# Kernel tuning notes

Hardware: AMD Instinct MI355X
Metric: run time of the kernel (lower is better)

The kernel has to match this reference:

```python
import jax, jax.numpy as jnp
import numpy as np

B, S, D = 4, 1024, 2048
H, KVH, HD = 32, 8, 64
N_REP = H // KVH  # 4
ROPE_THETA = 1000000.0


def _rope_tables(seq_len, head_dim, theta):
    inv_freq = 1.0 / (theta ** (np.arange(0, head_dim, 2, dtype=np.float32) / head_dim))
    t = np.arange(seq_len, dtype=np.float32)
    freqs = np.outer(t, inv_freq)                      # (S, HD/2)
    emb = np.concatenate([freqs, freqs], axis=-1)      # (S, HD)
    return jnp.asarray(np.cos(emb)), jnp.asarray(np.sin(emb))


def setup_inputs() -> dict:
    key = jax.random.key(0)
    kx, kq, kk, kv, ko = jax.random.split(key, 5)
    cos, sin = _rope_tables(S, HD, ROPE_THETA)
    s = 0.02
    return {
        "x": jax.random.normal(kx, (B, S, D), jnp.float32),
        "cos": cos,
        "sin": sin,
        "Wq": jax.random.normal(kq, (D, H * HD), jnp.float32) * s,
        "Wk": jax.random.normal(kk, (D, KVH * HD), jnp.float32) * s,
        "Wv": jax.random.normal(kv, (D, KVH * HD), jnp.float32) * s,
        "Wo": jax.random.normal(ko, (H * HD, D), jnp.float32) * s,
    }


def _rotate_half(t):
    t1, t2 = jnp.split(t, 2, axis=-1)
    return jnp.concatenate([-t2, t1], axis=-1)


def reference(x, cos, sin, Wq, Wk, Wv, Wo):
    # projections
    q = (x @ Wq).reshape(B, S, H, HD)      # (b, s, h, d)
    k = (x @ Wk).reshape(B, S, KVH, HD)
    v = (x @ Wv).reshape(B, S, KVH, HD)

    # RoPE: cos/sin (s, d) broadcast over heads (unsqueeze_dim=1 -> (s,1,d))
    c = cos[:, None, :]
    sn = sin[:, None, :]
    q = q * c + _rotate_half(q) * sn
    k = k * c + _rotate_half(k) * sn

    # GQA attention without physically repeating KV:
    # q grouped as (b, kvh, n_rep, s, d); repeat_kv '(h r)' maps q head g*n_rep+r -> kv head g
    qg = q.transpose(0, 2, 1, 3).reshape(B, KVH, N_REP, S, HD)
    kt = k.transpose(0, 2, 1, 3)  # (b, kvh, s, d)
    vt = v.transpose(0, 2, 1, 3)

    scale = 1.0 / jnp.sqrt(jnp.asarray(HD, x.dtype))
    scores = jnp.einsum('bgrqd,bgkd->bgrqk', qg, kt) * scale  # (b, kvh, rep, s, s)
    probs = jax.nn.softmax(scores, axis=-1)
    out = jnp.einsum('bgrqk,bgkd->bgrqd', probs, vt)           # (b, kvh, rep, s, d)

    out = out.reshape(B, H, S, HD).transpose(0, 2, 1, 3).reshape(B, S, H * HD)
    return out @ Wo
```

## Files before the change

### kernel.cpp

```cpp
#include <hip/hip_runtime.h>

typedef unsigned short u16;
typedef __attribute__((ext_vector_type(8))) __bf16 bf16x8;
typedef __attribute__((ext_vector_type(4))) _Float16 f16x4;
typedef __attribute__((ext_vector_type(8))) _Float16 f16x8;
typedef __attribute__((ext_vector_type(4))) float f32x4;

#define BB 4
#define SS 1024
#define DD 2048
#define HH 32
#define KVHN 8
#define HDIM 64

__device__ __forceinline__ u16 f2b(float f) {
    union { float f; unsigned u; } v; v.f = f;
    unsigned r = v.u + 0x7FFFu + ((v.u >> 16) & 1u);
    return (u16)(r >> 16);
}
__device__ __forceinline__ float b2f(u16 h) {
    union { unsigned u; float f; } v; v.u = ((unsigned)h) << 16; return v.f;
}

__device__ __forceinline__ f32x4 mfma16(bf16x8 a, bf16x8 b, f32x4 c) {
    return __builtin_amdgcn_mfma_f32_16x16x32_bf16(a, b, c, 0, 0, 0);
}
__device__ __forceinline__ f32x4 mfma16h(f16x8 a, f16x8 b, f32x4 c) {
    return __builtin_amdgcn_mfma_f32_16x16x32_f16(a, b, c, 0, 0, 0);
}

__device__ __forceinline__ void async_cp16(const void* g, void* l) {
    __builtin_amdgcn_global_load_lds((__attribute__((address_space(1))) void*)g,
                                     (__attribute__((address_space(3))) void*)l,
                                     16, 0, 0);
}

__device__ __forceinline__ void block_sync() {
    asm volatile("" ::: "memory");
    __builtin_amdgcn_s_barrier();
    asm volatile("" ::: "memory");
}

__device__ __forceinline__ f16x8 pack8_f16(const float* p) {
    union { unsigned u[4]; f16x8 v; } pu;
    pu.u[0] = __builtin_bit_cast(unsigned, __builtin_amdgcn_cvt_pkrtz(p[0], p[1]));
    pu.u[1] = __builtin_bit_cast(unsigned, __builtin_amdgcn_cvt_pkrtz(p[2], p[3]));
    pu.u[2] = __builtin_bit_cast(unsigned, __builtin_amdgcn_cvt_pkrtz(p[4], p[5]));
    pu.u[3] = __builtin_bit_cast(unsigned, __builtin_amdgcn_cvt_pkrtz(p[6], p[7]));
    return pu.v;
}

__global__ __launch_bounds__(256) void cast_x_kernel(const float* __restrict__ x,
                                                     u16* __restrict__ xb) {
    int i = (blockIdx.x * 256 + threadIdx.x) * 4;
    float4 v = *(const float4*)(x + i);
    unsigned r0 = (unsigned)f2b(v.x) | ((unsigned)f2b(v.y) << 16);
    unsigned r1 = (unsigned)f2b(v.z) | ((unsigned)f2b(v.w) << 16);
    *(uint2*)(xb + i) = make_uint2(r0, r1);
}

__global__ __launch_bounds__(256) void wtrans_all_kernel(const float* __restrict__ Wq,
                                                         const float* __restrict__ Wk,
                                                         const float* __restrict__ Wv,
                                                         const float* __restrict__ Wo,
                                                         u16* __restrict__ Wqkvt,
                                                         u16* __restrict__ Wot) {
    __shared__ float tile[32][33];
    int z = blockIdx.z;
    const float* W = (z == 0) ? Wq : (z == 1) ? Wk : (z == 2) ? Wv : Wo;
    int N = (z == 1 || z == 2) ? 512 : 2048;
    int n_off = (z == 1) ? 2048 : (z == 2) ? 2560 : 0;
    u16* Wt = (z == 3) ? Wot : Wqkvt;
    int n0 = blockIdx.x * 32;
    if (n0 >= N) return;
    int k0 = blockIdx.y * 32;
    int tid = threadIdx.x;
    int nj = tid & 31;
    int ki = tid >> 5;
#pragma unroll
    for (int it = 0; it < 4; it++) {
        int kk = it * 8 + ki;
        tile[kk][nj] = W[(size_t)(k0 + kk) * N + n0 + nj];
    }
    __syncthreads();
#pragma unroll
    for (int it = 0; it < 4; it++) {
        int nn = it * 8 + ki;
        Wt[(size_t)(n0 + nn + n_off) * 2048 + k0 + nj] = f2b(tile[nj][nn]);
    }
}

__global__ __launch_bounds__(512, 2) void gemm_qkv(const u16* __restrict__ A,
                                                   const u16* __restrict__ Bt,
                                                   u16* __restrict__ C) {
    __shared__ __align__(16) u16 Ls[4][16384];
    const int tid = threadIdx.x;
    const int lane = tid & 63;
    const int w = tid >> 6;
    const int m0 = blockIdx.y * 256;
    const int n0 = blockIdx.x * 256;
    const int wm = (w >> 2) * 128;
    const int wn = (w & 3) * 64;
    const int lr = lane & 15;
    const int lg = lane >> 4;

    const int srow = w * 16 + (lane >> 2);
    const int sg = (lane & 3) ^ ((srow >> 1) & 3);
    const u16* ap = A + (size_t)(m0 + srow) * 2048 + sg * 8;
    const u16* bp = Bt + (size_t)(n0 + srow) * 2048 + sg * 8;

#define QSTAGE_A(pb_, kt_)                                                       \
    {                                                                            \
        async_cp16(ap + (kt_) * 32, &Ls[pb_][0] + w * 512);                      \
        async_cp16(ap + (kt_) * 32 + 128 * 2048, &Ls[pb_][4096] + w * 512);      \
    }
#define QSTAGE_B(pb_, kt_)                                                       \
    {                                                                            \
        async_cp16(bp + (kt_) * 32, &Ls[pb_][8192] + w * 512);                   \
        async_cp16(bp + (kt_) * 32 + 128 * 2048, &Ls[pb_][12288] + w * 512);     \
    }

    f32x4 acc[8][4];
    const f32x4 zero4 = {0.f, 0.f, 0.f, 0.f};
#pragma unroll
    for (int i = 0; i < 8; i++)
#pragma unroll
        for (int j = 0; j < 4; j++) acc[i][j] = zero4;

    QSTAGE_A(0, 0); QSTAGE_B(0, 0);
    QSTAGE_A(1, 1); QSTAGE_B(1, 1);
    QSTAGE_A(2, 2); QSTAGE_B(2, 2);
    asm volatile("s_waitcnt vmcnt(8)" ::: "memory");
    block_sync();

#pragma unroll 4
    for (int t = 0; t < 64; ++t) {
        const int bufi = t & 3;
        const int pb = (t + 3) & 3;
        const int pt = (t + 3) & 63;
        const u16* Ab = &Ls[bufi][0];
        const u16* Bb = &Ls[bufi][8192];

        bf16x8 af[4], bfr[4];
#pragma unroll
        for (int ni = 0; ni < 4; ni++) {
            int r = wn + ni * 16 + lr;
            bfr[ni] = *(const bf16x8*)(Bb + r * 32 + ((lg ^ ((r >> 1) & 3)) * 8));
        }
#pragma unroll
        for (int mi = 0; mi < 4; mi++) {
            int r = wm + mi * 16 + lr;
            af[mi] = *(const bf16x8*)(Ab + r * 32 + ((lg ^ ((r >> 1) & 3)) * 8));
        }
        QSTAGE_A(pb, pt);
        __builtin_amdgcn_s_setprio(1);
#pragma unroll
        for (int mi = 0; mi < 4; mi++)
#pragma unroll
            for (int ni = 0; ni < 4; ni++)
                acc[mi][ni] = mfma16(af[mi], bfr[ni], acc[mi][ni]);
        __builtin_amdgcn_s_setprio(0);

#pragma unroll
        for (int mi = 0; mi < 4; mi++) {
            int r = wm + 64 + mi * 16 + lr;
            af[mi] = *(const bf16x8*)(Ab + r * 32 + ((lg ^ ((r >> 1) & 3)) * 8));
        }
        QSTAGE_B(pb, pt);
        __builtin_amdgcn_s_setprio(1);
#pragma unroll
        for (int mi = 0; mi < 4; mi++)
#pragma unroll
            for (int ni = 0; ni < 4; ni++)
                acc[4 + mi][ni] = mfma16(af[mi], bfr[ni], acc[4 + mi][ni]);
        __builtin_amdgcn_s_setprio(0);

        asm volatile("s_waitcnt vmcnt(8)" ::: "memory");
        block_sync();
    }
    asm volatile("s_waitcnt vmcnt(0)" ::: "memory");

    const int lq = lg * 4;
#pragma unroll
    for (int mi = 0; mi < 8; mi++)
#pragma unroll
        for (int ni = 0; ni < 4; ni++)
#pragma unroll
            for (int i = 0; i < 4; i++) {
                int r = m0 + wm + mi * 16 + lq + i;
                int c = n0 + wn + ni * 16 + lr;
                C[(size_t)r * 3072 + c] = f2b(acc[mi][ni][i]);
            }
#undef QSTAGE_A
#undef QSTAGE_B
}

__global__ __launch_bounds__(512, 2) void gemm_out(const u16* __restrict__ A,
                                                   const u16* __restrict__ Bt,
                                                   float* __restrict__ C) {
    __shared__ __align__(16) u16 Ls[4][12288];
    const int tid = threadIdx.x;
    const int lane = tid & 63;
    const int w = tid >> 6;
    const int m0 = blockIdx.y * 256;
    const int n0 = blockIdx.x * 128;
    const int wm = (w >> 1) * 64;
    const int wn = (w & 1) * 64;
    const int lr = lane & 15;
    const int lg = lane >> 4;

    const int srow = w * 16 + (lane >> 2);
    const int sg = (lane & 3) ^ ((srow >> 1) & 3);
    const u16* ap = A + (size_t)(m0 + srow) * 2048 + sg * 8;
    const u16* bp = Bt + (size_t)(n0 + srow) * 2048 + sg * 8;

#define OSTAGE(pb_, kt_)                                                         \
    {                                                                            \
        async_cp16(ap + (kt_) * 32, &Ls[pb_][0] + w * 512);                      \
        async_cp16(ap + (kt_) * 32 + 128 * 2048, &Ls[pb_][4096] + w * 512);      \
        async_cp16(bp + (kt_) * 32, &Ls[pb_][8192] + w * 512);                   \
    }

    f32x4 acc[4][4];
    const f32x4 zero4 = {0.f, 0.f, 0.f, 0.f};
#pragma unroll
    for (int i = 0; i < 4; i++)
#pragma unroll
        for (int j = 0; j < 4; j++) acc[i][j] = zero4;

    OSTAGE(0, 0);
    OSTAGE(1, 1);
    OSTAGE(2, 2);
    asm volatile("s_waitcnt vmcnt(6)" ::: "memory");
    block_sync();

#pragma unroll 4
    for (int t = 0; t < 64; ++t) {
        const int bufi = t & 3;
        const int pb = (t + 3) & 3;
        const int pt = (t + 3) & 63;
        const u16* Ab = &Ls[bufi][0];
        const u16* Bb = &Ls[bufi][8192];

        bf16x8 af[4], bfr[4];
#pragma unroll
        for (int ni = 0; ni < 4; ni++) {
            int r = wn + ni * 16 + lr;
            bfr[ni] = *(const bf16x8*)(Bb + r * 32 + ((lg ^ ((r >> 1) & 3)) * 8));
        }
#pragma unroll
        for (int mi = 0; mi < 4; mi++) {
            int r = wm + mi * 16 + lr;
            af[mi] = *(const bf16x8*)(Ab + r * 32 + ((lg ^ ((r >> 1) & 3)) * 8));
        }
        OSTAGE(pb, pt);
        __builtin_amdgcn_s_setprio(1);
#pragma unroll
        for (int mi = 0; mi < 4; mi++)
#pragma unroll
            for (int ni = 0; ni < 4; ni++)
                acc[mi][ni] = mfma16(af[mi], bfr[ni], acc[mi][ni]);
        __builtin_amdgcn_s_setprio(0);

        asm volatile("s_waitcnt vmcnt(6)" ::: "memory");
        block_sync();
    }
    asm volatile("s_waitcnt vmcnt(0)" ::: "memory");

    const int lq = lg * 4;
#pragma unroll
    for (int mi = 0; mi < 4; mi++)
#pragma unroll
        for (int ni = 0; ni < 4; ni++)
#pragma unroll
            for (int i = 0; i < 4; i++) {
                int r = m0 + wm + mi * 16 + lq + i;
                int c = n0 + wn + ni * 16 + lr;
                C[(size_t)r * 2048 + c] = acc[mi][ni][i];
            }
#undef OSTAGE
}

__global__ __launch_bounds__(256) void rope_kernel(const u16* __restrict__ QKV,
                                                   const float* __restrict__ cosT,
                                                   const float* __restrict__ sinT,
                                                   u16* __restrict__ Qh,
                                                   u16* __restrict__ Kh) {
    const float QSC = 0.125f * 1.44269504088896f;
    int idx = blockIdx.x * 256 + threadIdx.x;
    int d = idx & 31;
    int t = idx >> 5;
    int hh = t % 40;
    int row = t / 40;
    int s = row & (SS - 1);
    int b = row >> 10;
    float c = cosT[s * HDIM + d];
    float sn = sinT[s * HDIM + d];
    if (hh < 32) {
        const u16* src = QKV + (size_t)row * 3072 + hh * 64 + d;
        float x1 = b2f(src[0]), x2 = b2f(src[32]);
        u16* dst = Qh + ((size_t)(b * HH + hh) * SS + s) * 64 + d;
        dst[0] = f2b((x1 * c - x2 * sn) * QSC);
        dst[32] = f2b((x2 * c + x1 * sn) * QSC);
    } else {
        int g = hh - 32;
        const u16* src = QKV + (size_t)row * 3072 + 2048 + g * 64 + d;
        float x1 = b2f(src[0]), x2 = b2f(src[32]);
        int rr = s & 7;
        int kpos = (s & ~31) + ((rr >= 4) ? 16 : 0) + ((s >> 3) & 3) * 4 + (rr & 3);
        u16* dst = Kh + ((size_t)(b * KVHN + g) * SS + kpos) * 64 + d;
        dst[0] = f2b(x1 * c - x2 * sn);
        dst[32] = f2b(x2 * c + x1 * sn);
    }
}

__global__ __launch_bounds__(256) void vtrans_kernel(const u16* __restrict__ QKV,
                                                     u16* __restrict__ Vt) {
    __shared__ u16 tile[64][65];
    int blk = blockIdx.x;
    int st = blk & 15;
    int t2 = blk >> 4;
    int g = t2 & 7;
    int b = t2 >> 3;
    int tid = threadIdx.x;
    int cj = tid & 63;
    int ri = tid >> 6;
    const u16* src = QKV + ((size_t)(b * SS + st * 64)) * 3072 + 2560 + g * 64;
#pragma unroll
    for (int it = 0; it < 16; it++) {
        int s_i = it * 4 + ri;
        tile[s_i][cj] = src[(size_t)s_i * 3072 + cj];
    }
    __syncthreads();
    u16* dst = Vt + ((size_t)(b * KVHN + g) * HDIM) * SS + st * 64;
#pragma unroll
    for (int it = 0; it < 16; it++) {
        int hd_i = it * 4 + ri;
        _Float16 hv = (_Float16)b2f(tile[cj][hd_i]);
        union { _Float16 h; u16 u; } cv; cv.h = hv;
        dst[(size_t)hd_i * SS + cj] = cv.u;
    }
}

__global__ __launch_bounds__(256, 4) void flash_kernel(const u16* __restrict__ Qh,
                                                       const u16* __restrict__ Kh,
                                                       const u16* __restrict__ Vt,
                                                       u16* __restrict__ Attn) {
    __shared__ __align__(16) u16 Kls[2][4096];
    __shared__ __align__(16) u16 Vls[2][4096];
    const int tid = threadIdx.x;
    const int lane = tid & 63;
    const int w = tid >> 6;
    const int qt = blockIdx.x;
    const int g = blockIdx.y;
    const int b = blockIdx.z;
    const int h = g * 4 + w;
    const int lr = lane & 15;
    const int lg = lane >> 4;
    const int lk8 = lg * 8;
    const int lq = lg * 4;

    const u16* Qbase = Qh + ((size_t)(b * HH + h) * SS + qt * 32) * HDIM;
    bf16x8 qb[2][2];
#pragma unroll
    for (int j = 0; j < 2; j++) {
        qb[j][0] = *(const bf16x8*)(Qbase + (size_t)(j * 16 + lr) * HDIM + lk8);
        qb[j][1] = *(const bf16x8*)(Qbase + (size_t)(j * 16 + lr) * HDIM + 32 + lk8);
    }

    const u16* Kbase = Kh + (size_t)(b * KVHN + g) * SS * HDIM;
    const u16* Vbase = Vt + (size_t)(b * KVHN + g) * HDIM * SS;

    const int r0 = tid >> 3;
    const int c0 = tid & 7;

    const f32x4 zero4 = {0.f, 0.f, 0.f, 0.f};
    const f32x4 initS = {-4.f, -4.f, -4.f, -4.f};
    f32x4 o[2][4];
    float lsum[2] = {0.f, 0.f};
#pragma unroll
    for (int j = 0; j < 2; j++)
#pragma unroll
        for (int i = 0; i < 4; i++) o[j][i] = zero4;

#define STAGE(kt, p)                                                              \
    {                                                                             \
        _Pragma("unroll") for (int sh = 0; sh < 2; sh++) {                        \
            int rr = r0 + sh * 32;                                                \
            int cs = c0 ^ (rr & 7);                                               \
            async_cp16(Kbase + (size_t)((kt) + rr) * HDIM + cs * 8,               \
                       &Kls[p][sh * 2048 + w * 512]);                             \
            async_cp16(Vbase + (size_t)rr * SS + (kt) + cs * 8,                   \
                       &Vls[p][sh * 2048 + w * 512]);                             \
        }                                                                         \
    }

    STAGE(0, 0);
    __syncthreads();

    for (int t = 0; t < 16; t++) {
        const int p = t & 1;
        if (t < 15) STAGE((t + 1) * 64, p ^ 1);

#pragma unroll
        for (int c = 0; c < 2; c++) {
            f32x4 s[2][2];
#pragma unroll
            for (int halfi = 0; halfi < 2; halfi++) {
                const int R = c * 32 + halfi * 16 + lr;
                const u16* kr = &Kls[p][R * 64];
                bf16x8 kb0 = *(const bf16x8*)(kr + ((lg ^ (R & 7)) * 8));
                bf16x8 kb1 = *(const bf16x8*)(kr + (((4 + lg) ^ (R & 7)) * 8));
#pragma unroll
                for (int j = 0; j < 2; j++) {
                    f32x4 a = initS;
                    a = mfma16(kb0, qb[j][0], a);
                    a = mfma16(kb1, qb[j][1], a);
                    s[halfi][j] = a;
                }
            }

            f16x8 va[4];
#pragma unroll
            for (int hdt = 0; hdt < 4; hdt++) {
                const int R2 = hdt * 16 + lr;
                va[hdt] = *(const f16x8*)(&Vls[p][R2 * 64 + (((c * 4 + lg) ^ (R2 & 7)) * 8)]);
            }

#pragma unroll
            for (int j = 0; j < 2; j++) {
                float pv[8];
#pragma unroll
                for (int r = 0; r < 4; r++) {
                    pv[r] = __builtin_amdgcn_exp2f(s[0][j][r]);
                    pv[4 + r] = __builtin_amdgcn_exp2f(s[1][j][r]);
                }
                lsum[j] += ((pv[0] + pv[1]) + (pv[2] + pv[3])) +
                           ((pv[4] + pv[5]) + (pv[6] + pv[7]));
                f16x8 pb = pack8_f16(pv);
#pragma unroll
                for (int hdt = 0; hdt < 4; hdt++)
                    o[j][hdt] = mfma16h(va[hdt], pb, o[j][hdt]);
            }
        }
        __syncthreads();
    }

#pragma unroll
    for (int j = 0; j < 2; j++) {
        float su = lsum[j];
        su += __shfl_xor(su, 16);
        su += __shfl_xor(su, 32);
        float inv = 1.f / su;
        u16* Ob = Attn + ((size_t)(b * SS + qt * 32 + j * 16 + lr)) * 2048 + h * 64;
#pragma unroll
        for (int hdt = 0; hdt < 4; hdt++) {
            unsigned r0p = (unsigned)f2b(o[j][hdt][0] * inv) | ((unsigned)f2b(o[j][hdt][1] * inv) << 16);
            unsigned r1p = (unsigned)f2b(o[j][hdt][2] * inv) | ((unsigned)f2b(o[j][hdt][3] * inv) << 16);
            *(uint2*)(Ob + hdt * 16 + lq) = make_uint2(r0p, r1p);
        }
    }
}

extern "C" void kernel_launch(void* const* d_in, const int* in_sizes, int n_in,
                              void* d_out, int out_size, void* d_ws, size_t ws_size,
                              hipStream_t stream) {
    (void)in_sizes; (void)n_in; (void)out_size; (void)ws_size;
    const float* x = (const float*)d_in[0];
    const float* cosT = (const float*)d_in[1];
    const float* sinT = (const float*)d_in[2];
    const float* Wq = (const float*)d_in[3];
    const float* Wk = (const float*)d_in[4];
    const float* Wv = (const float*)d_in[5];
    const float* Wo = (const float*)d_in[6];
    float* out = (float*)d_out;

    char* ws = (char*)d_ws;
    u16* Xb    = (u16*)(ws);
    u16* Wqkvt = (u16*)(ws + 16777216);
    u16* Wot   = (u16*)(ws + 29360128);
    u16* QKV   = (u16*)(ws + 37748736);
    u16* Qh    = (u16*)(ws + 62914560);
    u16* Kh    = (u16*)(ws + 79691776);
    u16* Vt    = (u16*)(ws + 83886080);
    u16* Attn  = (u16*)(ws + 88080384);

    cast_x_kernel<<<8192, 256, 0, stream>>>(x, Xb);
    wtrans_all_kernel<<<dim3(64, 64, 4), 256, 0, stream>>>(Wq, Wk, Wv, Wo, Wqkvt, Wot);

    gemm_qkv<<<dim3(12, 16), 512, 0, stream>>>(Xb, Wqkvt, QKV);

    rope_kernel<<<20480, 256, 0, stream>>>(QKV, cosT, sinT, Qh, Kh);
    vtrans_kernel<<<512, 256, 0, stream>>>(QKV, Vt);

    flash_kernel<<<dim3(32, 8, 4), 256, 0, stream>>>(Qh, Kh, Vt, Attn);

    gemm_out<<<dim3(16, 16), 512, 0, stream>>>(Attn, Wot, out);
}
```

Baseline: 278.1 us.

## Retile GEMMs to smaller blocks with XCD-aware swizzled block mapping

The QKV and output GEMMs move from 512-thread blocks with large tiles (256x256, 256x128) to 256-thread blocks with 128x192 and 128x128 tiles, giving 512 blocks each to fill all CUs on the MI355X. Block indices are remapped so that blocks landing on the same XCD share M/N tile neighbourhoods for L2 reuse. The flash kernel also swaps to a 1D grid with an XCD-aware permutation of (batch, group, q-tile). Smaller tiles lower arithmetic intensity per block and add global traffic, traded for better occupancy and cache locality.

```diff
diff --git a/kernel.cpp b/kernel.cpp
--- a/kernel.cpp
+++ b/kernel.cpp
@@ -90,47 +90,55 @@
     }
 }
 
-__global__ __launch_bounds__(512, 2) void gemm_qkv(const u16* __restrict__ A,
+__global__ __launch_bounds__(256, 2) void gemm_qkv(const u16* __restrict__ A,
                                                    const u16* __restrict__ Bt,
                                                    u16* __restrict__ C) {
-    __shared__ __align__(16) u16 Ls[4][16384];
+    __shared__ __align__(16) u16 Ls[4][10240];
     const int tid = threadIdx.x;
     const int lane = tid & 63;
     const int w = tid >> 6;
-    const int m0 = blockIdx.y * 256;
-    const int n0 = blockIdx.x * 256;
-    const int wm = (w >> 2) * 128;
-    const int wn = (w & 3) * 64;
+
+    const int bid = blockIdx.x;
+    const int xcd = bid & 7;
+    const int loc = bid >> 3;
+    const int mt = (xcd & 3) * 8 + (loc & 7);
+    const int nt = (xcd >> 2) * 8 + (loc >> 3);
+    const int m0 = mt * 128;
+    const int n0 = nt * 192;
+
+    const int wm = (w >> 1) * 64;
+    const int wn = (w & 1) * 96;
     const int lr = lane & 15;
     const int lg = lane >> 4;
 
-    const int srow = w * 16 + (lane >> 2);
-    const int sg = (lane & 3) ^ ((srow >> 1) & 3);
-    const u16* ap = A + (size_t)(m0 + srow) * 2048 + sg * 8;
-    const u16* bp = Bt + (size_t)(n0 + srow) * 2048 + sg * 8;
-
-#define QSTAGE_A(pb_, kt_)                                                       \
-    {                                                                            \
-        async_cp16(ap + (kt_) * 32, &Ls[pb_][0] + w * 512);                      \
-        async_cp16(ap + (kt_) * 32 + 128 * 2048, &Ls[pb_][4096] + w * 512);      \
-    }
-#define QSTAGE_B(pb_, kt_)                                                       \
-    {                                                                            \
-        async_cp16(bp + (kt_) * 32, &Ls[pb_][8192] + w * 512);                   \
-        async_cp16(bp + (kt_) * 32 + 128 * 2048, &Ls[pb_][12288] + w * 512);     \
-    }
-
-    f32x4 acc[8][4];
+    const int srow = lane >> 2;
+    const int ar = w * 32 + srow;
+    const int ag = (lane & 3) ^ ((ar >> 1) & 3);
+    const u16* apA = A + (size_t)(m0 + ar) * 2048 + ag * 8;
+    const int br = w * 48 + srow;
+    const int bg = (lane & 3) ^ ((br >> 1) & 3);
+    const u16* apB = Bt + (size_t)(n0 + br) * 2048 + bg * 8;
+
+#define QSTAGE(pb_, kt_)                                                             \
+    {                                                                                \
+        async_cp16(apA + (kt_) * 32,             &Ls[pb_][w * 1024]);                \
+        async_cp16(apA + (kt_) * 32 + 16 * 2048, &Ls[pb_][w * 1024 + 512]);          \
+        async_cp16(apB + (kt_) * 32,             &Ls[pb_][4096 + w * 1536]);         \
+        async_cp16(apB + (kt_) * 32 + 16 * 2048, &Ls[pb_][4096 + w * 1536 + 512]);   \
+        async_cp16(apB + (kt_) * 32 + 32 * 2048, &Ls[pb_][4096 + w * 1536 + 1024]);  \
+    }
+
+    f32x4 acc[4][6];
     const f32x4 zero4 = {0.f, 0.f, 0.f, 0.f};
 #pragma unroll
-    for (int i = 0; i < 8; i++)
-#pragma unroll
-        for (int j = 0; j < 4; j++) acc[i][j] = zero4;
-
-    QSTAGE_A(0, 0); QSTAGE_B(0, 0);
-    QSTAGE_A(1, 1); QSTAGE_B(1, 1);
-    QSTAGE_A(2, 2); QSTAGE_B(2, 2);
-    asm volatile("s_waitcnt vmcnt(8)" ::: "memory");
+    for (int i = 0; i < 4; i++)
+#pragma unroll
+        for (int j = 0; j < 6; j++) acc[i][j] = zero4;
+
+    QSTAGE(0, 0);
+    QSTAGE(1, 1);
+    QSTAGE(2, 2);
+    asm volatile("s_waitcnt vmcnt(10)" ::: "memory");
     block_sync();
 
 #pragma unroll 4
@@ -139,11 +147,11 @@
         const int pb = (t + 3) & 3;
         const int pt = (t + 3) & 63;
         const u16* Ab = &Ls[bufi][0];
-        const u16* Bb = &Ls[bufi][8192];
-
-        bf16x8 af[4], bfr[4];
-#pragma unroll
-        for (int ni = 0; ni < 4; ni++) {
+        const u16* Bb = &Ls[bufi][4096];
+
+        bf16x8 bfr[6], af[4];
+#pragma unroll
+        for (int ni = 0; ni < 6; ni++) {
             int r = wn + ni * 16 + lr;
             bfr[ni] = *(const bf16x8*)(Bb + r * 32 + ((lg ^ ((r >> 1) & 3)) * 8));
         }
@@ -152,73 +160,67 @@
             int r = wm + mi * 16 + lr;
             af[mi] = *(const bf16x8*)(Ab + r * 32 + ((lg ^ ((r >> 1) & 3)) * 8));
         }
-        QSTAGE_A(pb, pt);
+        QSTAGE(pb, pt);
         __builtin_amdgcn_s_setprio(1);
 #pragma unroll
         for (int mi = 0; mi < 4; mi++)
 #pragma unroll
-            for (int ni = 0; ni < 4; ni++)
+            for (int ni = 0; ni < 6; ni++)
                 acc[mi][ni] = mfma16(af[mi], bfr[ni], acc[mi][ni]);
         __builtin_amdgcn_s_setprio(0);
 
-#pragma unroll
-        for (int mi = 0; mi < 4; mi++) {
-            int r = wm + 64 + mi * 16 + lr;
-            af[mi] = *(const bf16x8*)(Ab + r * 32 + ((lg ^ ((r >> 1) & 3)) * 8));
-        }
-        QSTAGE_B(pb, pt);
-        __builtin_amdgcn_s_setprio(1);
-#pragma unroll
-        for (int mi = 0; mi < 4; mi++)
-#pragma unroll
-            for (int ni = 0; ni < 4; ni++)
-                acc[4 + mi][ni] = mfma16(af[mi], bfr[ni], acc[4 + mi][ni]);
-        __builtin_amdgcn_s_setprio(0);
-
-        asm volatile("s_waitcnt vmcnt(8)" ::: "memory");
+        asm volatile("s_waitcnt vmcnt(10)" ::: "memory");
         block_sync();
     }
     asm volatile("s_waitcnt vmcnt(0)" ::: "memory");
 
     const int lq = lg * 4;
 #pragma unroll
-    for (int mi = 0; mi < 8; mi++)
-#pragma unroll
-        for (int ni = 0; ni < 4; ni++)
+    for (int mi = 0; mi < 4; mi++)
+#pragma unroll
+        for (int ni = 0; ni < 6; ni++)
 #pragma unroll
             for (int i = 0; i < 4; i++) {
                 int r = m0 + wm + mi * 16 + lq + i;
                 int c = n0 + wn + ni * 16 + lr;
                 C[(size_t)r * 3072 + c] = f2b(acc[mi][ni][i]);
             }
-#undef QSTAGE_A
-#undef QSTAGE_B
-}
-
-__global__ __launch_bounds__(512, 2) void gemm_out(const u16* __restrict__ A,
+#undef QSTAGE
+}
+
+__global__ __launch_bounds__(256, 2) void gemm_out(const u16* __restrict__ A,
                                                    const u16* __restrict__ Bt,
                                                    float* __restrict__ C) {
-    __shared__ __align__(16) u16 Ls[4][12288];
+    __shared__ __align__(16) u16 Ls[4][8192];
     const int tid = threadIdx.x;
     const int lane = tid & 63;
     const int w = tid >> 6;
-    const int m0 = blockIdx.y * 256;
-    const int n0 = blockIdx.x * 128;
+
+    const int bid = blockIdx.x;
+    const int xcd = bid & 7;
+    const int loc = bid >> 3;
+    const int mt = (xcd & 3) * 8 + (loc & 7);
+    const int nt = (xcd >> 2) * 8 + (loc >> 3);
+    const int m0 = mt * 128;
+    const int n0 = nt * 128;
+
     const int wm = (w >> 1) * 64;
     const int wn = (w & 1) * 64;
     const int lr = lane & 15;
     const int lg = lane >> 4;
 
-    const int srow = w * 16 + (lane >> 2);
-    const int sg = (lane & 3) ^ ((srow >> 1) & 3);
-    const u16* ap = A + (size_t)(m0 + srow) * 2048 + sg * 8;
-    const u16* bp = Bt + (size_t)(n0 + srow) * 2048 + sg * 8;
-
-#define OSTAGE(pb_, kt_)                                                         \
-    {                                                                            \
-        async_cp16(ap + (kt_) * 32, &Ls[pb_][0] + w * 512);                      \
-        async_cp16(ap + (kt_) * 32 + 128 * 2048, &Ls[pb_][4096] + w * 512);      \
-        async_cp16(bp + (kt_) * 32, &Ls[pb_][8192] + w * 512);                   \
+    const int srow = lane >> 2;
+    const int ar = w * 32 + srow;
+    const int ag = (lane & 3) ^ ((ar >> 1) & 3);
+    const u16* apA = A + (size_t)(m0 + ar) * 2048 + ag * 8;
+    const u16* apB = Bt + (size_t)(n0 + ar) * 2048 + ag * 8;
+
+#define OSTAGE(pb_, kt_)                                                             \
+    {                                                                                \
+        async_cp16(apA + (kt_) * 32,             &Ls[pb_][w * 1024]);                \
+        async_cp16(apA + (kt_) * 32 + 16 * 2048, &Ls[pb_][w * 1024 + 512]);          \
+        async_cp16(apB + (kt_) * 32,             &Ls[pb_][4096 + w * 1024]);         \
+        async_cp16(apB + (kt_) * 32 + 16 * 2048, &Ls[pb_][4096 + w * 1024 + 512]);   \
     }
 
     f32x4 acc[4][4];
@@ -231,7 +233,7 @@
     OSTAGE(0, 0);
     OSTAGE(1, 1);
     OSTAGE(2, 2);
-    asm volatile("s_waitcnt vmcnt(6)" ::: "memory");
+    asm volatile("s_waitcnt vmcnt(8)" ::: "memory");
     block_sync();
 
 #pragma unroll 4
@@ -240,9 +242,9 @@
         const int pb = (t + 3) & 3;
         const int pt = (t + 3) & 63;
         const u16* Ab = &Ls[bufi][0];
-        const u16* Bb = &Ls[bufi][8192];
-
-        bf16x8 af[4], bfr[4];
+        const u16* Bb = &Ls[bufi][4096];
+
+        bf16x8 bfr[4], af[4];
 #pragma unroll
         for (int ni = 0; ni < 4; ni++) {
             int r = wn + ni * 16 + lr;
@@ -262,7 +264,7 @@
                 acc[mi][ni] = mfma16(af[mi], bfr[ni], acc[mi][ni]);
         __builtin_amdgcn_s_setprio(0);
 
-        asm volatile("s_waitcnt vmcnt(6)" ::: "memory");
+        asm volatile("s_waitcnt vmcnt(8)" ::: "memory");
         block_sync();
     }
     asm volatile("s_waitcnt vmcnt(0)" ::: "memory");
@@ -351,9 +353,11 @@
     const int tid = threadIdx.x;
     const int lane = tid & 63;
     const int w = tid >> 6;
-    const int qt = blockIdx.x;
-    const int g = blockIdx.y;
-    const int b = blockIdx.z;
+    const int bid = blockIdx.x;
+    const int gbp = ((bid & 7) << 2) | ((bid >> 3) & 3);
+    const int qt = bid >> 5;
+    const int g = gbp & 7;
+    const int b = gbp >> 3;
     const int h = g * 4 + w;
     const int lr = lane & 15;
     const int lg = lane >> 4;
@@ -387,7 +391,7 @@
     {                                                                             \
         _Pragma("unroll") for (int sh = 0; sh < 2; sh++) {                        \
             int rr = r0 + sh * 32;                                                \
-            int cs = c0 ^ (rr & 7);                                               \
+            int cs = c0 ^ (rr & 7);                                              \
             async_cp16(Kbase + (size_t)((kt) + rr) * HDIM + cs * 8,               \
                        &Kls[p][sh * 2048 + w * 512]);                             \
             async_cp16(Vbase + (size_t)rr * SS + (kt) + cs * 8,                   \
@@ -488,12 +492,12 @@
     cast_x_kernel<<<8192, 256, 0, stream>>>(x, Xb);
     wtrans_all_kernel<<<dim3(64, 64, 4), 256, 0, stream>>>(Wq, Wk, Wv, Wo, Wqkvt, Wot);
 
-    gemm_qkv<<<dim3(12, 16), 512, 0, stream>>>(Xb, Wqkvt, QKV);
+    gemm_qkv<<<512, 256, 0, stream>>>(Xb, Wqkvt, QKV);
 
     rope_kernel<<<20480, 256, 0, stream>>>(QKV, cosT, sinT, Qh, Kh);
     vtrans_kernel<<<512, 256, 0, stream>>>(QKV, Vt);
 
-    flash_kernel<<<dim3(32, 8, 4), 256, 0, stream>>>(Qh, Kh, Vt, Attn);
-
-    gemm_out<<<dim3(16, 16), 512, 0, stream>>>(Attn, Wot, out);
-}
+    flash_kernel<<<1024, 256, 0, stream>>>(Qh, Kh, Vt, Attn);
+
+    gemm_out<<<512, 256, 0, stream>>>(Attn, Wot, out);
+}
```

Result: no change. 278.9 us (+0.3%).
